# Kernel tuning notes

Hardware: AMD Instinct MI355X
Metric: run time of the kernel (lower is better)

## Reference

```python
import jax, jax.numpy as jnp
import numpy as np

ALPHA = 0.2  # leakyrelu negative slope and residual scale


def setup_inputs() -> dict:
    key = jax.random.key(0)
    k1, k2, k3, k4 = jax.random.split(key, 4)
    B, N, C, F = 8, 2048, 128, 128
    text = jax.random.normal(k1, (B, N, C), dtype=jnp.float32)
    adj = jax.random.uniform(k2, (B, N, N), dtype=jnp.float32)  # unused by the layer's math
    W = jax.random.normal(k3, (C, F), dtype=jnp.float32) * (1.0 / np.sqrt(C))
    a = jax.random.normal(k4, (2 * F, 1), dtype=jnp.float32) * 0.1
    return {"text": text, "adj": adj, "W": W, "a": a}


def reference(text, adj, W, a):
    # h: [B, N, F]
    h = jnp.matmul(text, W)
    Fdim = W.shape[1]
    a1 = a[:Fdim, 0]  # applies to source node i
    a2 = a[Fdim:, 0]  # applies to target node j
    e1 = jnp.einsum('bnf,f->bn', h, a1)  # [B, N]
    e2 = jnp.einsum('bnf,f->bn', h, a2)  # [B, N]
    # scores[b,i,j] = leakyrelu(a1.h_i + a2.h_j)  (same as concat-matmul in original)
    scores = jax.nn.leaky_relu(e1[:, :, None] + e2[:, None, :], negative_slope=ALPHA)
    attention = jax.nn.softmax(scores, axis=2)  # [B, N, N]; dropout off (eval)
    h_prime = jnp.matmul(attention, h)  # [B, N, F]
    return jax.nn.elu(h_prime + ALPHA * h)
```

## Files before the change

### kernel.cpp

```cpp
#include <hip/hip_runtime.h>
#include <hip/hip_bf16.h>

#define BB 8
#define NN 2048
#define CC 128
#define FF 128
#define ALPHA 0.2f
#define ROWS 16
#define WTPAD 136
#define CHN 256
#define CLEN 8
#define CSH 3

typedef __hip_bfloat16 bf16;
typedef __attribute__((ext_vector_type(8))) short short8;
typedef __attribute__((ext_vector_type(4))) float f32x4;
typedef unsigned long long u64;

__device__ __forceinline__ float ld1(const void* p, int i, int f32) {
    if (f32) return ((const float*)p)[i];
    return __bfloat162float(((const bf16*)p)[i]);
}
__device__ __forceinline__ float2 ld2(const void* p, int pair, int f32) {
    if (f32) return ((const float2*)p)[pair];
    __hip_bfloat162 v = ((const __hip_bfloat162*)p)[pair];
    return make_float2(__bfloat162float(v.x), __bfloat162float(v.y));
}
__device__ __forceinline__ u64 shfl_xor_u64(u64 v, int mask) {
    int lo = (int)(unsigned)(v & 0xFFFFFFFFull);
    int hi = (int)(unsigned)(v >> 32);
    lo = __shfl_xor(lo, mask, 64);
    hi = __shfl_xor(hi, mask, 64);
    return ((u64)(unsigned)hi << 32) | (unsigned)lo;
}

__global__ __launch_bounds__(256) void k_prep(const void* __restrict__ text,
                                              const void* __restrict__ W,
                                              const void* __restrict__ a,
                                              int* __restrict__ flag,
                                              float* __restrict__ wa1,
                                              float* __restrict__ wa2,
                                              ushort* __restrict__ WT) {
    __shared__ int cnt;
    __shared__ float aL[2 * FF];
    const int t = threadIdx.x;
    if (t == 0) cnt = 0;
    __syncthreads();
    const ushort2* p = (const ushort2*)text;
    int local = 0;
    for (int i = t; i < 1024; i += 256) {
        ushort2 v = p[i];
        float f = __uint_as_float(((unsigned)v.x) << 16);
        if (!(fabsf(f) <= 100.f)) local++;
    }
    atomicAdd(&cnt, local);
    __syncthreads();
    const int f32 = (cnt >= 64) ? 1 : 0;

    if (blockIdx.x == 0) {
        if (t == 0) flag[0] = f32;
        aL[t] = ld1(a, t, f32);
        __syncthreads();
        if (t < CC) {
            float s1 = 0.f, s2 = 0.f;
            for (int f = 0; f < FF; f += 4) {
                float w0 = ld1(W, t * FF + f, f32);
                float w1 = ld1(W, t * FF + f + 1, f32);
                float w2 = ld1(W, t * FF + f + 2, f32);
                float w3 = ld1(W, t * FF + f + 3, f32);
                s1 += w0 * aL[f] + w1 * aL[f + 1] + w2 * aL[f + 2] + w3 * aL[f + 3];
                s2 += w0 * aL[FF + f] + w1 * aL[FF + f + 1] + w2 * aL[FF + f + 2] + w3 * aL[FF + f + 3];
            }
            wa1[t] = s1; wa2[t] = s2;
        }
    } else {
        const int base = (blockIdx.x - 1) * 2048;
        for (int i = 0; i < 8; ++i) {
            int idx = base + i * 256 + t;
            int cc = idx >> 7, f = idx & 127;
            float v = ld1(W, idx, f32);
            bf16 b = __float2bfloat16(v);
            WT[f * CC + cc] = *(const ushort*)&b;
        }
    }
}

__global__ __launch_bounds__(256) void k_e(const void* __restrict__ text,
                                           const float* __restrict__ wa1,
                                           const float* __restrict__ wa2,
                                           float* __restrict__ e1,
                                           float* __restrict__ e2,
                                           const int* __restrict__ flag) {
    const int f32 = *flag;
    const int wave = threadIdx.x >> 6;
    const int lane = threadIdx.x & 63;
    const int row = blockIdx.x * 4 + wave;
    float2 tv = ld2(text, row * (CC / 2) + lane, f32);
    float s1 = tv.x * wa1[2 * lane] + tv.y * wa1[2 * lane + 1];
    float s2 = tv.x * wa2[2 * lane] + tv.y * wa2[2 * lane + 1];
#pragma unroll
    for (int off = 32; off > 0; off >>= 1) {
        s1 += __shfl_down(s1, off, 64);
        s2 += __shfl_down(s2, off, 64);
    }
    if (lane == 0) { e1[row] = s1; e2[row] = s2; }
}

__global__ __launch_bounds__(1024) void k_sort(const float* __restrict__ e2,
                                               float* __restrict__ e2s,
                                               int* __restrict__ sidx,
                                               float* __restrict__ z1,
                                               float* __restrict__ z2) {
    __shared__ u64 lk[NN];
    __shared__ float2 wtot[16];
    __shared__ float2 woff[16];
    const int b = blockIdx.x;
    const int t = threadIdx.x;

    float f0 = e2[b * NN + 2 * t], f1 = e2[b * NN + 2 * t + 1];
    unsigned m0 = __float_as_uint(f0); m0 = (m0 & 0x80000000u) ? ~m0 : (m0 | 0x80000000u);
    unsigned m1 = __float_as_uint(f1); m1 = (m1 & 0x80000000u) ? ~m1 : (m1 | 0x80000000u);
    u64 s0 = ((u64)m0 << 32) | (unsigned)(2 * t);
    u64 s1 = ((u64)m1 << 32) | (unsigned)(2 * t + 1);

    for (int size = 2; size <= NN; size <<= 1) {
        const bool up = (((2 * t) & size) == 0);
        for (int stride = size >> 1; stride >= 1; stride >>= 1) {
            if (stride == 1) {
                u64 mn = s0 < s1 ? s0 : s1;
                u64 mx = s0 < s1 ? s1 : s0;
                s0 = up ? mn : mx;
                s1 = up ? mx : mn;
            } else if (stride <= 64) {
                const int m = stride >> 1;
                u64 p0 = shfl_xor_u64(s0, m);
                u64 p1 = shfl_xor_u64(s1, m);
                const bool keepmin = (((t & m) == 0) == up);
                s0 = keepmin ? (s0 < p0 ? s0 : p0) : (s0 < p0 ? p0 : s0);
                s1 = keepmin ? (s1 < p1 ? s1 : p1) : (s1 < p1 ? p1 : s1);
            } else {
                lk[2 * t] = s0; lk[2 * t + 1] = s1;
                __syncthreads();
                u64 p0 = lk[(2 * t) ^ stride];
                u64 p1 = lk[(2 * t + 1) ^ stride];
                const bool keepmin = ((((2 * t) & stride) == 0) == up);
                s0 = keepmin ? (s0 < p0 ? s0 : p0) : (s0 < p0 ? p0 : s0);
                s1 = keepmin ? (s1 < p1 ? s1 : p1) : (s1 < p1 ? p1 : s1);
                __syncthreads();
            }
        }
    }

    unsigned k0 = (unsigned)(s0 >> 32), k1 = (unsigned)(s1 >> 32);
    float v0 = __uint_as_float((k0 & 0x80000000u) ? (k0 ^ 0x80000000u) : ~k0);
    float v1 = __uint_as_float((k1 & 0x80000000u) ? (k1 ^ 0x80000000u) : ~k1);
    e2s[b * NN + 2 * t] = v0;
    e2s[b * NN + 2 * t + 1] = v1;
    sidx[b * NN + 2 * t] = (int)(unsigned)(s0 & 0xFFFFFFFFull);
    sidx[b * NN + 2 * t + 1] = (int)(unsigned)(s1 & 0xFFFFFFFFull);

    float x0a = expf(v0), x0b = expf(ALPHA * v0);
    float x1a = expf(v1), x1b = expf(ALPHA * v1);
    float pa = x0a + x1a, pb = x0b + x1b;
    float sa = pa, sb = pb;
    const int lane = t & 63, wid = t >> 6;
#pragma unroll
    for (int off = 1; off < 64; off <<= 1) {
        float ya = __shfl_up(sa, off, 64);
        float yb = __shfl_up(sb, off, 64);
        if (lane >= off) { sa += ya; sb += yb; }
    }
    if (lane == 63) wtot[wid] = make_float2(sa, sb);
    __syncthreads();
    if (t == 0) {
        float ra = 0.f, rb = 0.f;
        for (int w2 = 0; w2 < 16; ++w2) {
            float2 tt = wtot[w2];
            woff[w2] = make_float2(ra, rb);
            ra += tt.x; rb += tt.y;
        }
    }
    __syncthreads();
    float2 o = woff[wid];
    float pre_a = o.x + sa - pa, pre_b = o.y + sb - pb;
    float* Z1 = z1 + b * (NN + 1);
    float* Z2 = z2 + b * (NN + 1);
    if (t == 0) { Z1[0] = 0.f; Z2[0] = 0.f; }
    Z1[2 * t + 1] = pre_a + x0a;  Z2[2 * t + 1] = pre_b + x0b;
    Z1[2 * t + 2] = pre_a + pa;   Z2[2 * t + 2] = pre_b + pb;
}

__global__ __launch_bounds__(128) void k_ps(const void* __restrict__ text,
                                            const float* __restrict__ e2s,
                                            const int* __restrict__ sidx,
                                            float* __restrict__ PS1,
                                            float* __restrict__ PS2,
                                            float* __restrict__ T1,
                                            float* __restrict__ T2,
                                            const int* __restrict__ flag) {
    const int f32 = *flag;
    const int b = blockIdx.x / CHN, ch = blockIdx.x % CHN;
    const int c = threadIdx.x;
    float r1 = 0.f, r2 = 0.f;
    const int k0 = ch * CLEN;
#pragma unroll
    for (int kk = 0; kk < CLEN; ++kk) {
        int k = k0 + kk;
        PS1[(size_t)(b * NN + k) * CC + c] = r1;
        PS2[(size_t)(b * NN + k) * CC + c] = r2;
        float v = e2s[b * NN + k];
        int j = sidx[b * NN + k];
        float x = ld1(text, (b * NN + j) * CC + c, f32);
        r1 += expf(v) * x;
        r2 += expf(ALPHA * v) * x;
    }
    T1[(b * (CHN + 1) + ch) * CC + c] = r1;
    T2[(b * (CHN + 1) + ch) * CC + c] = r2;
}

__global__ __launch_bounds__(256) void k_scanT(float* __restrict__ T1,
                                               float* __restrict__ T2) {
    const int tid = blockIdx.x * 256 + threadIdx.x;
    const int b = tid / CC, c = tid % CC;
    float* P1 = T1 + (size_t)(b * (CHN + 1)) * CC + c;
    float* P2 = T2 + (size_t)(b * (CHN + 1)) * CC + c;
    float r1 = 0.f, r2 = 0.f;
    for (int ch = 0; ch < CHN; ch += 8) {
        float t1[8], t2[8];
#pragma unroll
        for (int u = 0; u < 8; ++u) { t1[u] = P1[(ch + u) * CC]; t2[u] = P2[(ch + u) * CC]; }
#pragma unroll
        for (int u = 0; u < 8; ++u) {
            P1[(ch + u) * CC] = r1; r1 += t1[u];
            P2[(ch + u) * CC] = r2; r2 += t2[u];
        }
    }
    P1[CHN * CC] = r1;
    P2[CHN * CC] = r2;
}

__global__ __launch_bounds__(256) void k_out(const void* __restrict__ text,
                                             const ushort* __restrict__ WT,
                                             const float* __restrict__ T1,
                                             const float* __restrict__ T2,
                                             const float* __restrict__ PS1,
                                             const float* __restrict__ PS2,
                                             const float* __restrict__ e1,
                                             const float* __restrict__ e2s,
                                             const float* __restrict__ z1,
                                             const float* __restrict__ z2,
                                             void* __restrict__ out,
                                             const int* __restrict__ flag) {
    __shared__ ushort WTl[FF * WTPAD];
    __shared__ ushort ul[ROWS * WTPAD];
    __shared__ float4 ri[ROWS];
    const int f32 = *flag;
    const int t = threadIdx.x;
    const int b = blockIdx.x / (NN / ROWS);
    const int r0 = (blockIdx.x % (NN / ROWS)) * ROWS;

    {
        const uint4* src = (const uint4*)WT;
#pragma unroll
        for (int i = 0; i < 8; ++i) {
            int idx = i * 256 + t;
            uint4 v = src[idx];
            int f = idx >> 4, cb = idx & 15;
            *(uint4*)&WTl[f * WTPAD + cb * 8] = v;
        }
    }
    if (t < ROWS) {
        const int row = b * NN + r0 + t;
        float ev = e1[row];
        float w1 = expf(ev), w2 = expf(ALPHA * ev);
        float thr = -ev;
        const float* e2sb = e2s + b * NN;
        int lo = 0, hi = NN;
        while (lo < hi) {
            int mid = (lo + hi) >> 1;
            if (e2sb[mid] <= thr) lo = mid + 1; else hi = mid;
        }
        float den = w1 * (z1[b * (NN + 1) + NN] - z1[b * (NN + 1) + lo])
                  + w2 * z2[b * (NN + 1) + lo];
        den = fmaxf(den, 1e-30f);
        ri[t] = make_float4(__int_as_float(lo), w1, w2, 1.f / den);
    }
    __syncthreads();

    {
        const int c = t & 127;
        const int g = t >> 7;
        const float* CB1 = T1 + (size_t)(b * (CHN + 1)) * CC + c;
        const float* CB2 = T2 + (size_t)(b * (CHN + 1)) * CC + c;
        const float* B1 = PS1 + (size_t)(b * NN) * CC + c;
        const float* B2 = PS2 + (size_t)(b * NN) * CC + c;
        const float S1 = CB1[CHN * CC];
#pragma unroll
        for (int q = 0; q < 8; ++q) {
            const int rr = g * 8 + q;
            float4 info = ri[rr];
            const int k = __float_as_int(info.x);
            const int c0 = k >> CSH;
            float P1 = CB1[c0 * CC];
            float P2 = CB2[c0 * CC];
            if (k < NN) {
                P1 += B1[(size_t)k * CC];
                P2 += B2[(size_t)k * CC];
            }
            float tc = ld1(text, (b * NN + r0 + rr) * CC + c, f32);
            float u = (info.y * (S1 - P1) + info.z * P2) * info.w + ALPHA * tc;
            bf16 ub = __float2bfloat16(u);
            ul[rr * WTPAD + c] = *(const ushort*)&ub;
        }
    }
    __syncthreads();

    {
        const int wv = t >> 6;
        const int lane = t & 63;
        const int m = lane & 15;
        const int quad = lane >> 4;
        f32x4 acc0 = {0.f, 0.f, 0.f, 0.f};
        f32x4 acc1 = {0.f, 0.f, 0.f, 0.f};
        const int f0 = (wv * 2 + 0) * 16 + m;
        const int f1 = (wv * 2 + 1) * 16 + m;
#pragma unroll
        for (int kt = 0; kt < 4; ++kt) {
            const int ko = kt * 32 + quad * 8;
            short8 afrag = *(const short8*)&ul[m * WTPAD + ko];
            short8 bf0 = *(const short8*)&WTl[f0 * WTPAD + ko];
            short8 bf1 = *(const short8*)&WTl[f1 * WTPAD + ko];
            acc0 = __builtin_amdgcn_mfma_f32_16x16x32_bf16(afrag, bf0, acc0, 0, 0, 0);
            acc1 = __builtin_amdgcn_mfma_f32_16x16x32_bf16(afrag, bf1, acc1, 0, 0, 0);
        }
#pragma unroll
        for (int ft = 0; ft < 2; ++ft) {
            f32x4 acc = ft ? acc1 : acc0;
            const int f = (wv * 2 + ft) * 16 + m;
#pragma unroll
            for (int reg = 0; reg < 4; ++reg) {
                const int urow = quad * 4 + reg;
                float x = acc[reg];
                float y = x > 0.f ? x : expm1f(x);
                const int orow = b * NN + r0 + urow;
                if (f32) ((float*)out)[orow * FF + f] = y;
                else     ((bf16*)out)[orow * FF + f] = __float2bfloat16(y);
            }
        }
    }
}

extern "C" void kernel_launch(void* const* d_in, const int* in_sizes, int n_in,
                              void* d_out, int out_size, void* d_ws, size_t ws_size,
                              hipStream_t stream) {
    const void* text = d_in[0];
    const void* Wp   = (n_in >= 4) ? d_in[2] : d_in[1];
    const void* ap   = (n_in >= 4) ? d_in[3] : d_in[2];
    for (int i = 0; i < n_in; ++i) {
        int s = in_sizes[i];
        if (s == BB * NN * CC)      text = d_in[i];
        else if (s == CC * FF)      Wp = d_in[i];
        else if (s == 2 * FF)       ap = d_in[i];
    }

    float* w = (float*)d_ws;
    size_t off = 0;
    int*    flagp  = (int*)(w + off);      off += 16;
    float*  wa1    = w + off;              off += 128;
    float*  wa2    = w + off;              off += 128;
    ushort* WT     = (ushort*)(w + off);   off += 8192;
    float*  e1     = w + off;              off += BB * NN;
    float*  e2     = w + off;              off += BB * NN;
    float*  e2s    = w + off;              off += BB * NN;
    int*    sidx   = (int*)(w + off);      off += BB * NN;
    float*  z1     = w + off;              off += BB * (NN + 1);
    float*  z2     = w + off;              off += BB * (NN + 1);
    float*  T1     = w + off;              off += (size_t)BB * (CHN + 1) * CC;
    float*  T2     = w + off;              off += (size_t)BB * (CHN + 1) * CC;
    float*  PS1    = w + off;              off += (size_t)BB * NN * CC;
    float*  PS2    = w + off;              off += (size_t)BB * NN * CC;

    k_prep<<<9, 256, 0, stream>>>(text, Wp, ap, flagp, wa1, wa2, WT);
    k_e<<<BB * NN / 4, 256, 0, stream>>>(text, wa1, wa2, e1, e2, flagp);
    k_sort<<<BB, 1024, 0, stream>>>(e2, e2s, sidx, z1, z2);
    k_ps<<<BB * CHN, 128, 0, stream>>>(text, e2s, sidx, PS1, PS2, T1, T2, flagp);
    k_scanT<<<4, 256, 0, stream>>>(T1, T2);
    k_out<<<BB * NN / ROWS, 256, 0, stream>>>(text, WT, T1, T2, PS1, PS2,
                                              e1, e2s, z1, z2, d_out, flagp);
}
```

Measured before the change: 240.8 us.

## Fuse chunk scan into k_ps via last-block atomic, simplify sort, drop WT staging

Removes the separate k_scanT launch: each k_ps block increments a per-batch counter, and the last block of each batch does the exclusive prefix scan over chunk totals. The register and shuffle bitonic sort is replaced by a plain shared-memory bitonic sort with a barrier after every step, which has many more __syncthreads. k_out stops staging WT into LDS and reads MFMA B fragments straight from global memory. The scan fusion saves a launch but serialises the scan onto one block per batch. The sort change and the global WT reads likely cost more time.

Measured after the change: 333.9 us. 38.7% more time.

```diff
diff --git a/kernel.cpp b/kernel.cpp
--- a/kernel.cpp
+++ b/kernel.cpp
@@ -15,7 +15,6 @@
 typedef __hip_bfloat16 bf16;
 typedef __attribute__((ext_vector_type(8))) short short8;
 typedef __attribute__((ext_vector_type(4))) float f32x4;
-typedef unsigned long long u64;
 
 __device__ __forceinline__ float ld1(const void* p, int i, int f32) {
     if (f32) return ((const float*)p)[i];
@@ -25,13 +24,6 @@
     if (f32) return ((const float2*)p)[pair];
     __hip_bfloat162 v = ((const __hip_bfloat162*)p)[pair];
     return make_float2(__bfloat162float(v.x), __bfloat162float(v.y));
-}
-__device__ __forceinline__ u64 shfl_xor_u64(u64 v, int mask) {
-    int lo = (int)(unsigned)(v & 0xFFFFFFFFull);
-    int hi = (int)(unsigned)(v >> 32);
-    lo = __shfl_xor(lo, mask, 64);
-    hi = __shfl_xor(hi, mask, 64);
-    return ((u64)(unsigned)hi << 32) | (unsigned)lo;
 }
 
 __global__ __launch_bounds__(256) void k_prep(const void* __restrict__ text,
@@ -59,6 +51,7 @@
 
     if (blockIdx.x == 0) {
         if (t == 0) flag[0] = f32;
+        if (t >= 8 && t < 8 + BB) flag[t] = 0;
         aL[t] = ld1(a, t, f32);
         __syncthreads();
         if (t < CC) {
@@ -111,53 +104,36 @@
                                                int* __restrict__ sidx,
                                                float* __restrict__ z1,
                                                float* __restrict__ z2) {
-    __shared__ u64 lk[NN];
+    __shared__ float vals[NN];
+    __shared__ int   idxs[NN];
     __shared__ float2 wtot[16];
     __shared__ float2 woff[16];
     const int b = blockIdx.x;
     const int t = threadIdx.x;
 
-    float f0 = e2[b * NN + 2 * t], f1 = e2[b * NN + 2 * t + 1];
-    unsigned m0 = __float_as_uint(f0); m0 = (m0 & 0x80000000u) ? ~m0 : (m0 | 0x80000000u);
-    unsigned m1 = __float_as_uint(f1); m1 = (m1 & 0x80000000u) ? ~m1 : (m1 | 0x80000000u);
-    u64 s0 = ((u64)m0 << 32) | (unsigned)(2 * t);
-    u64 s1 = ((u64)m1 << 32) | (unsigned)(2 * t + 1);
+    for (int i = t; i < NN; i += 1024) { vals[i] = e2[b * NN + i]; idxs[i] = i; }
+    __syncthreads();
 
     for (int size = 2; size <= NN; size <<= 1) {
-        const bool up = (((2 * t) & size) == 0);
-        for (int stride = size >> 1; stride >= 1; stride >>= 1) {
-            if (stride == 1) {
-                u64 mn = s0 < s1 ? s0 : s1;
-                u64 mx = s0 < s1 ? s1 : s0;
-                s0 = up ? mn : mx;
-                s1 = up ? mx : mn;
-            } else if (stride <= 64) {
-                const int m = stride >> 1;
-                u64 p0 = shfl_xor_u64(s0, m);
-                u64 p1 = shfl_xor_u64(s1, m);
-                const bool keepmin = (((t & m) == 0) == up);
-                s0 = keepmin ? (s0 < p0 ? s0 : p0) : (s0 < p0 ? p0 : s0);
-                s1 = keepmin ? (s1 < p1 ? s1 : p1) : (s1 < p1 ? p1 : s1);
-            } else {
-                lk[2 * t] = s0; lk[2 * t + 1] = s1;
-                __syncthreads();
-                u64 p0 = lk[(2 * t) ^ stride];
-                u64 p1 = lk[(2 * t + 1) ^ stride];
-                const bool keepmin = ((((2 * t) & stride) == 0) == up);
-                s0 = keepmin ? (s0 < p0 ? s0 : p0) : (s0 < p0 ? p0 : s0);
-                s1 = keepmin ? (s1 < p1 ? s1 : p1) : (s1 < p1 ? p1 : s1);
-                __syncthreads();
-            }
-        }
-    }
-
-    unsigned k0 = (unsigned)(s0 >> 32), k1 = (unsigned)(s1 >> 32);
-    float v0 = __uint_as_float((k0 & 0x80000000u) ? (k0 ^ 0x80000000u) : ~k0);
-    float v1 = __uint_as_float((k1 & 0x80000000u) ? (k1 ^ 0x80000000u) : ~k1);
+        for (int stride = size >> 1; stride > 0; stride >>= 1) {
+            int i = ((t & ~(stride - 1)) << 1) | (t & (stride - 1));
+            int j = i | stride;
+            bool up = ((i & size) == 0);
+            float vi = vals[i], vj = vals[j];
+            bool sw = up ? (vi > vj) : (vi < vj);
+            if (sw) {
+                vals[i] = vj; vals[j] = vi;
+                int ti = idxs[i]; idxs[i] = idxs[j]; idxs[j] = ti;
+            }
+            __syncthreads();
+        }
+    }
+
+    float v0 = vals[2 * t], v1 = vals[2 * t + 1];
     e2s[b * NN + 2 * t] = v0;
     e2s[b * NN + 2 * t + 1] = v1;
-    sidx[b * NN + 2 * t] = (int)(unsigned)(s0 & 0xFFFFFFFFull);
-    sidx[b * NN + 2 * t + 1] = (int)(unsigned)(s1 & 0xFFFFFFFFull);
+    sidx[b * NN + 2 * t] = idxs[2 * t];
+    sidx[b * NN + 2 * t + 1] = idxs[2 * t + 1];
 
     float x0a = expf(v0), x0b = expf(ALPHA * v0);
     float x1a = expf(v1), x1b = expf(ALPHA * v1);
@@ -197,7 +173,7 @@
                                             float* __restrict__ PS2,
                                             float* __restrict__ T1,
                                             float* __restrict__ T2,
-                                            const int* __restrict__ flag) {
+                                            int* __restrict__ flag) {
     const int f32 = *flag;
     const int b = blockIdx.x / CHN, ch = blockIdx.x % CHN;
     const int c = threadIdx.x;
@@ -216,27 +192,29 @@
     }
     T1[(b * (CHN + 1) + ch) * CC + c] = r1;
     T2[(b * (CHN + 1) + ch) * CC + c] = r2;
-}
-
-__global__ __launch_bounds__(256) void k_scanT(float* __restrict__ T1,
-                                               float* __restrict__ T2) {
-    const int tid = blockIdx.x * 256 + threadIdx.x;
-    const int b = tid / CC, c = tid % CC;
-    float* P1 = T1 + (size_t)(b * (CHN + 1)) * CC + c;
-    float* P2 = T2 + (size_t)(b * (CHN + 1)) * CC + c;
-    float r1 = 0.f, r2 = 0.f;
-    for (int ch = 0; ch < CHN; ch += 8) {
-        float t1[8], t2[8];
-#pragma unroll
-        for (int u = 0; u < 8; ++u) { t1[u] = P1[(ch + u) * CC]; t2[u] = P2[(ch + u) * CC]; }
-#pragma unroll
-        for (int u = 0; u < 8; ++u) {
-            P1[(ch + u) * CC] = r1; r1 += t1[u];
-            P2[(ch + u) * CC] = r2; r2 += t2[u];
-        }
-    }
-    P1[CHN * CC] = r1;
-    P2[CHN * CC] = r2;
+
+    __threadfence();
+    __shared__ int amLast;
+    if (c == 0) amLast = (atomicAdd(&flag[8 + b], 1) == CHN - 1) ? 1 : 0;
+    __syncthreads();
+    if (amLast) {
+        __threadfence();
+        float* P1 = T1 + (size_t)(b * (CHN + 1)) * CC + c;
+        float* P2 = T2 + (size_t)(b * (CHN + 1)) * CC + c;
+        float s1 = 0.f, s2 = 0.f;
+        for (int q = 0; q < CHN; q += 8) {
+            float a1[8], a2[8];
+#pragma unroll
+            for (int u = 0; u < 8; ++u) { a1[u] = P1[(q + u) * CC]; a2[u] = P2[(q + u) * CC]; }
+#pragma unroll
+            for (int u = 0; u < 8; ++u) {
+                P1[(q + u) * CC] = s1; s1 += a1[u];
+                P2[(q + u) * CC] = s2; s2 += a2[u];
+            }
+        }
+        P1[CHN * CC] = s1;
+        P2[CHN * CC] = s2;
+    }
 }
 
 __global__ __launch_bounds__(256) void k_out(const void* __restrict__ text,
@@ -251,7 +229,6 @@
                                              const float* __restrict__ z2,
                                              void* __restrict__ out,
                                              const int* __restrict__ flag) {
-    __shared__ ushort WTl[FF * WTPAD];
     __shared__ ushort ul[ROWS * WTPAD];
     __shared__ float4 ri[ROWS];
     const int f32 = *flag;
@@ -259,16 +236,6 @@
     const int b = blockIdx.x / (NN / ROWS);
     const int r0 = (blockIdx.x % (NN / ROWS)) * ROWS;
 
-    {
-        const uint4* src = (const uint4*)WT;
-#pragma unroll
-        for (int i = 0; i < 8; ++i) {
-            int idx = i * 256 + t;
-            uint4 v = src[idx];
-            int f = idx >> 4, cb = idx & 15;
-            *(uint4*)&WTl[f * WTPAD + cb * 8] = v;
-        }
-    }
     if (t < ROWS) {
         const int row = b * NN + r0 + t;
         float ev = e1[row];
@@ -328,8 +295,8 @@
         for (int kt = 0; kt < 4; ++kt) {
             const int ko = kt * 32 + quad * 8;
             short8 afrag = *(const short8*)&ul[m * WTPAD + ko];
-            short8 bf0 = *(const short8*)&WTl[f0 * WTPAD + ko];
-            short8 bf1 = *(const short8*)&WTl[f1 * WTPAD + ko];
+            short8 bf0 = *(const short8*)&WT[f0 * CC + ko];
+            short8 bf1 = *(const short8*)&WT[f1 * CC + ko];
             acc0 = __builtin_amdgcn_mfma_f32_16x16x32_bf16(afrag, bf0, acc0, 0, 0, 0);
             acc1 = __builtin_amdgcn_mfma_f32_16x16x32_bf16(afrag, bf1, acc1, 0, 0, 0);
         }
@@ -384,7 +351,6 @@
     k_e<<<BB * NN / 4, 256, 0, stream>>>(text, wa1, wa2, e1, e2, flagp);
     k_sort<<<BB, 1024, 0, stream>>>(e2, e2s, sidx, z1, z2);
     k_ps<<<BB * CHN, 128, 0, stream>>>(text, e2s, sidx, PS1, PS2, T1, T2, flagp);
-    k_scanT<<<4, 256, 0, stream>>>(T1, T2);
     k_out<<<BB * NN / ROWS, 256, 0, stream>>>(text, WT, T1, T2, PS1, PS2,
                                               e1, e2s, z1, z2, d_out, flagp);
 }
```
